# Kernel optimization log

Measured on AMD Instinct MI355X. Metric: run time of the kernel, lower is better.

Reference implementation:

```python
import jax, jax.numpy as jnp
import numpy as np

B, S, D, H, F, M = 2, 2048, 1024, 16, 4096, 1024
HD = D // H
LR, MOM_DECAY, WD, THRESH = 0.01, 0.9, 0.01, 0.1


def rmsnorm(x, w, eps=1e-8):
    n = jnp.linalg.norm(x, axis=-1, keepdims=True) * (x.shape[-1] ** -0.5)
    return w * x / (n + eps)


def rope_sin_cos(seq_len, dim):
    inv_freq = 1.0 / (10000.0 ** (jnp.arange(0, dim, 2, dtype=jnp.float32) / dim))
    ang = jnp.arange(seq_len, dtype=jnp.float32)[:, None] * inv_freq[None, :]  # [S, dim/2]
    return jnp.sin(ang), jnp.cos(ang)


def apply_rope(x, sin, cos):
    # x: [B,H,S,hd]; sin/cos: [S,hd/2] broadcast. Matches torch source:
    # split even/odd lanes, then CONCATENATE halves (not interleave).
    x1, x2 = x[..., ::2], x[..., 1::2]
    return jnp.concatenate([x1 * cos - x2 * sin, x1 * sin + x2 * cos], axis=-1)


def lmm_mlp(z, w0, b0, w1, b1):
    return jnp.maximum(z @ w0 + b0, 0.0) @ w1 + b1


def setup_inputs() -> dict:
    key = jax.random.key(0)
    k = jax.random.split(key, 20)
    sc = 0.02
    r = lambda i, shape: jax.random.normal(k[i], shape, jnp.float32) * sc
    return {
        'x': jax.random.normal(k[0], (B, S, D), jnp.float32),
        'mask': jnp.tril(jnp.ones((1, 1, S, S), dtype=bool)),
        'wq': r(1, (D, D)), 'wk': r(2, (D, D)), 'wv': r(3, (D, D)), 'wo': r(4, (D, D)),
        'n1': jnp.ones(D, jnp.float32), 'n2': jnp.ones(D, jnp.float32), 'n3': jnp.ones(D, jnp.float32),
        'ffn_w1': r(5, (D, F)), 'ffn_w2': r(6, (D, F)), 'ffn_w3': r(7, (F, D)),
        'pk_w': r(8, (D, M)), 'pk_b': jnp.zeros(M, jnp.float32),
        'pv_w': r(9, (D, M)), 'pv_b': jnp.zeros(M, jnp.float32),
        'pq_w': r(10, (D, M)), 'pq_b': jnp.zeros(M, jnp.float32),
        'l0_w': r(11, (M, M)), 'l0_b': jnp.zeros(M, jnp.float32),
        'l1_w': r(12, (M, M)), 'l1_b': jnp.zeros(M, jnp.float32),
        'm0_w': jnp.zeros((M, M), jnp.float32), 'm0_b': jnp.zeros(M, jnp.float32),
        'm1_w': jnp.zeros((M, M), jnp.float32), 'm1_b': jnp.zeros(M, jnp.float32),
    }


def reference(x, mask, wq, wk, wv, wo, n1, n2, n3, ffn_w1, ffn_w2, ffn_w3,
              pk_w, pk_b, pv_w, pv_b, pq_w, pq_b,
              l0_w, l0_b, l1_w, l1_b, m0_w, m0_b, m1_w, m1_b):
    # ---- attention sublayer (pre-norm, RoPE) ----
    hn = rmsnorm(x, n1)
    q = (hn @ wq).reshape(B, S, H, HD).transpose(0, 2, 1, 3)
    kk = (hn @ wk).reshape(B, S, H, HD).transpose(0, 2, 1, 3)
    v = (hn @ wv).reshape(B, S, H, HD).transpose(0, 2, 1, 3)
    sin, cos = rope_sin_cos(S, HD)
    q = apply_rope(q, sin, cos)
    kk = apply_rope(kk, sin, cos)
    scores = jnp.einsum('bhqd,bhkd->bhqk', q, kk) / np.sqrt(HD).astype(np.float32)
    scores = jnp.where(mask, scores, -jnp.inf)
    attn = jax.nn.softmax(scores, axis=-1)
    o = jnp.einsum('bhqk,bhkd->bhqd', attn, v).transpose(0, 2, 1, 3).reshape(B, S, D)
    h = x + o @ wo

    # ---- neural memory sublayer ----
    hn2 = rmsnorm(h, n2)
    q_lmm = hn2 @ pq_w + pq_b
    retrieved = lmm_mlp(q_lmm, l0_w, l0_b, l1_w, l1_b)  # uses PRE-update params

    # online Titan-style LMM update (torch does this under no_grad, after retrieval)
    kf = jax.lax.stop_gradient((hn2 @ pk_w + pk_b).reshape(B * S, M))
    vf = jax.lax.stop_gradient((hn2 @ pv_w + pv_b).reshape(B * S, M))

    def lmm_loss(params):
        pred = lmm_mlp(kf, *params)
        return jnp.sum(jnp.mean((pred - vf) ** 2, axis=-1))

    params = (l0_w, l0_b, l1_w, l1_b)
    loss_sum, grads = jax.value_and_grad(lmm_loss)(params)
    avg_loss = loss_sum / (B * S)
    do_update = avg_loss >= THRESH
    moms = (m0_w, m0_b, m1_w, m1_b)
    new_moms, new_params = [], []
    for p, m, g in zip(params, moms, grads):
        nm = MOM_DECAY * m - LR * g
        np_ = p * (1.0 - WD) + nm
        new_moms.append(jnp.where(do_update, nm, m))
        new_params.append(jnp.where(do_update, np_, p))

    h = h + retrieved

    # ---- SwiGLU FFN sublayer ----
    hn3 = rmsnorm(h, n3)
    ffn = (jax.nn.silu(hn3 @ ffn_w1) * (hn3 @ ffn_w2)) @ ffn_w3
    out = h + ffn
    return (out, *new_params, *new_moms)
```

## Files before the change

kernel.cpp:

```cpp
#include <hip/hip_runtime.h>
#include <cstdint>
#include <cstddef>

typedef __bf16 bf16;
typedef __bf16 bf16x2 __attribute__((ext_vector_type(2)));
typedef __bf16 bf16x4 __attribute__((ext_vector_type(4)));
typedef __bf16 bf16x8 __attribute__((ext_vector_type(8)));
typedef float  f32x4  __attribute__((ext_vector_type(4)));
typedef float  f32x16 __attribute__((ext_vector_type(16)));
typedef __attribute__((address_space(1))) unsigned int u32_g;
typedef __attribute__((address_space(3))) unsigned int u32_l;

#define DI __device__ __forceinline__

constexpr int Bc = 2, Sc = 2048, Dc = 1024, Hc = 16, HDc = 64, Fc = 4096, Mc = 1024;
constexpr int NTc = Bc * Sc;

DI void llds16(const bf16* g, bf16* l) {
  __builtin_amdgcn_global_load_lds((const u32_g*)g, (u32_l*)l, 16, 0, 0);
}
DI f32x4 cvt4(bf16x4 a) {
  f32x4 r; r[0] = (float)a[0]; r[1] = (float)a[1]; r[2] = (float)a[2]; r[3] = (float)a[3];
  return r;
}

__global__ void k_detect(const unsigned short* __restrict__ x, int* __restrict__ flag)
{
  const int tid = threadIdx.x;
  int cnt = 0;
#pragma unroll
  for (int i = 0; i < 8; i++) {
    unsigned short h = x[tid * 8 + i];
    int e = (h >> 7) & 0xFF;
    if (e < 96 || e > 160) cnt++;
  }
#pragma unroll
  for (int off = 32; off > 0; off >>= 1) cnt += __shfl_down(cnt, off, 64);
  if (tid == 0) *flag = (cnt > 32) ? 1 : 0;
}

__global__ __launch_bounds__(256)
void k_cvt(const void* __restrict__ src, bf16* __restrict__ dst, int n4, const int* __restrict__ flag)
{
  int i = blockIdx.x * 256 + threadIdx.x;
  if (i >= n4) return;
  bf16x4 o;
  if (*flag) {
    f32x4 v = ((const f32x4*)src)[i];
    o[0] = (bf16)v[0]; o[1] = (bf16)v[1]; o[2] = (bf16)v[2]; o[3] = (bf16)v[3];
  } else {
    o = ((const bf16x4*)src)[i];
  }
  ((bf16x4*)dst)[i] = o;
}

__global__ void k_transpose_dt(const void* __restrict__ src, bf16* __restrict__ dst,
                               int R, int C, const int* __restrict__ flag)
{
  __shared__ bf16 tile[32][33];
  const int c0 = blockIdx.x * 32, r0 = blockIdx.y * 32;
  const int tx = threadIdx.x, ty = threadIdx.y;
  const bool f32 = (*flag != 0);
  for (int i = ty; i < 32; i += 8) {
    size_t idx = (size_t)(r0 + i) * C + (c0 + tx);
    tile[i][tx] = f32 ? (bf16)((const float*)src)[idx] : ((const bf16*)src)[idx];
  }
  __syncthreads();
  for (int i = ty; i < 32; i += 8)
    dst[(size_t)(c0 + i) * R + (r0 + tx)] = tile[tx][i];
}

__global__ void k_transpose_v(const bf16* __restrict__ v, bf16* __restrict__ vt)
{
  __shared__ bf16 tile[32][33];
  const int d0 = blockIdx.x * 32, s0 = blockIdx.y * 32;
  const int bh = blockIdx.z;
  const int b = bh >> 4, hh = bh & 15;
  const int tx = threadIdx.x, ty = threadIdx.y;
  for (int i = ty; i < 32; i += 8)
    tile[i][tx] = v[((size_t)(b * Sc + s0 + i)) * Dc + hh * HDc + d0 + tx];
  __syncthreads();
  for (int i = ty; i < 32; i += 8)
    vt[((size_t)(bh * HDc + d0 + i)) * Sc + s0 + tx] = tile[tx][i];
}

enum EpiMode { EPI_BF16 = 0, EPI_BIAS_BF16, EPI_BIAS_RELU_BF16, EPI_BIAS_RESB_F32,
               EPI_SILU_BF16, EPI_DZ_BF16, EPI_RESX_BF16, EPI_RESF_F32,
               EPI_SEGC_BF16, EPI_SEGC_BIAS_BF16, EPI_SEG2_RELU_BF16, EPI_ATOMIC_F32 };

template <int EPI>
__global__ __launch_bounds__(256)
void k_gemm(const bf16* __restrict__ A, const bf16* __restrict__ Bt,
            int Mr, int Nr, int Kr,
            float* outF, bf16* outB,
            const bf16* __restrict__ bias, const bf16* auxB,
            const float* resF,
            const void* __restrict__ resX, const int* __restrict__ flag)
{
  __shared__ bf16 As[128 * 32];
  __shared__ bf16 Bs[128 * 32];
  const int tid = threadIdx.x;
  const int w = tid >> 6, l = tid & 63;
  const int wr = w >> 1, wc = w & 1;
  const int row0 = blockIdx.y * 128, col0 = blockIdx.x * 128;

  const f32x4 vzero = {0.f, 0.f, 0.f, 0.f};
  f32x4 acc[4][4];
#pragma unroll
  for (int i = 0; i < 4; i++)
#pragma unroll
    for (int j = 0; j < 4; j++) acc[i][j] = vzero;

  const bf16* Ag = A + (size_t)(row0 + w * 16 + (l >> 2)) * Kr + ((l & 3) << 3);
  const bf16* Bg = Bt + (size_t)(col0 + w * 16 + (l >> 2)) * Kr + ((l & 3) << 3);
  bf16* AsW = &As[w * 512];
  bf16* BsW = &Bs[w * 512];
  const size_t rowHop = (size_t)64 * Kr;

  const int chunk = Kr / gridDim.z;
  const int kbeg = blockIdx.z * chunk;

  for (int k0 = kbeg; k0 < kbeg + chunk; k0 += 32) {
    __syncthreads();
    llds16(Ag + k0, AsW);
    llds16(Ag + rowHop + k0, AsW + 2048);
    llds16(Bg + k0, BsW);
    llds16(Bg + rowHop + k0, BsW + 2048);
    __syncthreads();
    bf16x8 af[4], bfr[4];
#pragma unroll
    for (int mt = 0; mt < 4; mt++)
      af[mt] = *(const bf16x8*)&As[(wr * 64 + mt * 16 + (l & 15)) * 32 + (l >> 4) * 8];
#pragma unroll
    for (int nt = 0; nt < 4; nt++)
      bfr[nt] = *(const bf16x8*)&Bs[(wc * 64 + nt * 16 + (l & 15)) * 32 + (l >> 4) * 8];
#pragma unroll
    for (int mt = 0; mt < 4; mt++)
#pragma unroll
      for (int nt = 0; nt < 4; nt++)
        acc[mt][nt] = __builtin_amdgcn_mfma_f32_16x16x32_bf16(af[mt], bfr[nt], acc[mt][nt], 0, 0, 0);
  }

  const bool f32res = (EPI == EPI_RESX_BF16) ? (*flag != 0) : false;
  float biasv[4];
  if (EPI == EPI_BIAS_BF16 || EPI == EPI_BIAS_RELU_BF16 || EPI == EPI_BIAS_RESB_F32 ||
      EPI == EPI_SEGC_BIAS_BF16 || EPI == EPI_SEG2_RELU_BF16) {
#pragma unroll
    for (int nt = 0; nt < 4; nt++)
      biasv[nt] = (float)bias[col0 + wc * 64 + nt * 16 + (l & 15)];
  }
#pragma unroll
  for (int mt = 0; mt < 4; mt++) {
    const int rowb = row0 + wr * 64 + mt * 16 + ((l >> 4) << 2);
    float av[4][4];
    if (EPI == EPI_SILU_BF16 || EPI == EPI_DZ_BF16 || EPI == EPI_BIAS_RESB_F32) {
#pragma unroll
      for (int nt = 0; nt < 4; nt++) {
        const int col = col0 + wc * 64 + nt * 16 + (l & 15);
#pragma unroll
        for (int r = 0; r < 4; r++)
          av[nt][r] = (float)auxB[(size_t)(rowb + r) * Nr + col];
      }
    }
    if (EPI == EPI_RESF_F32) {
#pragma unroll
      for (int nt = 0; nt < 4; nt++) {
        const int col = col0 + wc * 64 + nt * 16 + (l & 15);
#pragma unroll
        for (int r = 0; r < 4; r++)
          av[nt][r] = resF[(size_t)(rowb + r) * Nr + col];
      }
    }
    if (EPI == EPI_RESX_BF16) {
#pragma unroll
      for (int nt = 0; nt < 4; nt++) {
        const int col = col0 + wc * 64 + nt * 16 + (l & 15);
#pragma unroll
        for (int r = 0; r < 4; r++) {
          const size_t idx = (size_t)(rowb + r) * Nr + col;
          av[nt][r] = f32res ? ((const float*)resX)[idx] : (float)((const bf16*)resX)[idx];
        }
      }
    }
#pragma unroll
    for (int nt = 0; nt < 4; nt++) {
      const int col = col0 + wc * 64 + nt * 16 + (l & 15);
#pragma unroll
      for (int r = 0; r < 4; r++) {
        const size_t idx = (size_t)(rowb + r) * Nr + col;
        float v = acc[mt][nt][r];
        if (EPI == EPI_BF16) { outB[idx] = (bf16)v; }
        else if (EPI == EPI_BIAS_BF16) { outB[idx] = (bf16)(v + biasv[nt]); }
        else if (EPI == EPI_BIAS_RELU_BF16) { outB[idx] = (bf16)fmaxf(v + biasv[nt], 0.f); }
        else if (EPI == EPI_BIAS_RESB_F32) { outF[idx] = v + biasv[nt] + av[nt][r]; }
        else if (EPI == EPI_SILU_BF16) {
          float s1v = av[nt][r];
          float sl = s1v / (1.f + __expf(-s1v));
          outB[idx] = (bf16)(sl * v);
        }
        else if (EPI == EPI_DZ_BF16) { outB[idx] = (bf16)(av[nt][r] > 0.f ? v : 0.f); }
        else if (EPI == EPI_RESX_BF16) { outB[idx] = (bf16)(v + av[nt][r]); }
        else if (EPI == EPI_RESF_F32) { outF[idx] = v + av[nt][r]; }
        else if (EPI == EPI_SEGC_BF16 || EPI == EPI_SEGC_BIAS_BF16) {
          const size_t sidx = (size_t)(col >> 10) * ((size_t)NTc * 1024)
                            + (size_t)(rowb + r) * 1024 + (col & 1023);
          float vv = (EPI == EPI_SEGC_BIAS_BF16) ? (v + biasv[nt]) : v;
          outB[sidx] = (bf16)vv;
        }
        else if (EPI == EPI_SEG2_RELU_BF16) {
          bf16* ob = (rowb >> 12) ? (bf16*)outF : outB;
          ob[(size_t)((rowb + r) & 4095) * 1024 + col] = (bf16)fmaxf(v + biasv[nt], 0.f);
        }
        else if (EPI == EPI_ATOMIC_F32) {
          atomicAdd(&outF[(size_t)(rowb + r) * Nr + col], v);
        }
      }
    }
  }
}

__global__ __launch_bounds__(256)
void k_gemm_tn(const bf16* __restrict__ X, const bf16* __restrict__ Y, int Kt,
               float* __restrict__ out)
{
  __shared__ bf16 As[128 * 36];
  __shared__ bf16 Bs[128 * 36];
  const int tid = threadIdx.x;
  const int w = tid >> 6, l = tid & 63;
  const int wr = w >> 1, wc = w & 1;
  const int row0 = blockIdx.y * 128, col0 = blockIdx.x * 128;
  const int iofs = (tid & 15) * 8;
  const int tp   = (tid >> 4) * 2;

  const f32x4 vzero = {0.f, 0.f, 0.f, 0.f};
  f32x4 acc[4][4];
#pragma unroll
  for (int i = 0; i < 4; i++)
#pragma unroll
    for (int j = 0; j < 4; j++) acc[i][j] = vzero;

  const int chunk = Kt / gridDim.z;
  const int tbeg = blockIdx.z * chunk;

  for (int t0 = tbeg; t0 < tbeg + chunk; t0 += 32) {
    __syncthreads();
    bf16x8 a0 = *(const bf16x8*)&X[(size_t)(t0 + tp) * 1024 + row0 + iofs];
    bf16x8 a1 = *(const bf16x8*)&X[(size_t)(t0 + tp + 1) * 1024 + row0 + iofs];
    bf16x8 b0 = *(const bf16x8*)&Y[(size_t)(t0 + tp) * 1024 + col0 + iofs];
    bf16x8 b1 = *(const bf16x8*)&Y[(size_t)(t0 + tp + 1) * 1024 + col0 + iofs];
#pragma unroll
    for (int e = 0; e < 8; e++) {
      bf16x2 pa; pa[0] = a0[e]; pa[1] = a1[e];
      bf16x2 pb; pb[0] = b0[e]; pb[1] = b1[e];
      *(bf16x2*)&As[(iofs + e) * 36 + tp] = pa;
      *(bf16x2*)&Bs[(iofs + e) * 36 + tp] = pb;
    }
    __syncthreads();
    bf16x8 af[4], bfr[4];
#pragma unroll
    for (int mt = 0; mt < 4; mt++) {
      const int base = (wr * 64 + mt * 16 + (l & 15)) * 36 + (l >> 4) * 8;
      bf16x4 lo = *(const bf16x4*)&As[base];
      bf16x4 hi = *(const bf16x4*)&As[base + 4];
#pragma unroll
      for (int e = 0; e < 4; e++) { af[mt][e] = lo[e]; af[mt][4 + e] = hi[e]; }
    }
#pragma unroll
    for (int nt = 0; nt < 4; nt++) {
      const int base = (wc * 64 + nt * 16 + (l & 15)) * 36 + (l >> 4) * 8;
      bf16x4 lo = *(const bf16x4*)&Bs[base];
      bf16x4 hi = *(const bf16x4*)&Bs[base + 4];
#pragma unroll
      for (int e = 0; e < 4; e++) { bfr[nt][e] = lo[e]; bfr[nt][4 + e] = hi[e]; }
    }
#pragma unroll
    for (int mt = 0; mt < 4; mt++)
#pragma unroll
      for (int nt = 0; nt < 4; nt++)
        acc[mt][nt] = __builtin_amdgcn_mfma_f32_16x16x32_bf16(af[mt], bfr[nt], acc[mt][nt], 0, 0, 0);
  }

#pragma unroll
  for (int mt = 0; mt < 4; mt++) {
    const int rowb = row0 + wr * 64 + mt * 16 + ((l >> 4) << 2);
#pragma unroll
    for (int nt = 0; nt < 4; nt++) {
      const int col = col0 + wc * 64 + nt * 16 + (l & 15);
#pragma unroll
      for (int r = 0; r < 4; r++)
        atomicAdd(&out[(size_t)(rowb + r) * 1024 + col], acc[mt][nt][r]);
    }
  }
}

__global__ __launch_bounds__(256)
void k_rmsnorm_dt(const void* __restrict__ x, const bf16* __restrict__ w, bf16* __restrict__ out,
                  const int* __restrict__ flag)
{
  const int row = blockIdx.x;
  const int tid = threadIdx.x;
  f32x4 xv;
  if (*flag) xv = *(const f32x4*)((const float*)x + (size_t)row * Dc + tid * 4);
  else       xv = cvt4(*(const bf16x4*)((const bf16*)x + (size_t)row * Dc + tid * 4));
  float ss = xv[0] * xv[0] + xv[1] * xv[1] + xv[2] * xv[2] + xv[3] * xv[3];
#pragma unroll
  for (int off = 32; off > 0; off >>= 1) ss += __shfl_down(ss, off, 64);
  __shared__ float part[4];
  if ((tid & 63) == 0) part[tid >> 6] = ss;
  __syncthreads();
  float tot = part[0] + part[1] + part[2] + part[3];
  float inv = 1.f / (sqrtf(tot) * 0.03125f + 1e-8f);
  bf16x4 wb = *(const bf16x4*)(w + tid * 4);
  bf16x4 ov;
  ov[0] = (bf16)((float)wb[0] * xv[0] * inv);
  ov[1] = (bf16)((float)wb[1] * xv[1] * inv);
  ov[2] = (bf16)((float)wb[2] * xv[2] * inv);
  ov[3] = (bf16)((float)wb[3] * xv[3] * inv);
  *(bf16x4*)(out + (size_t)row * Dc + tid * 4) = ov;
}

__global__ __launch_bounds__(256)
void k_rmsnorm_b(const bf16* __restrict__ x, const bf16* __restrict__ w, bf16* __restrict__ out)
{
  const int row = blockIdx.x;
  const int tid = threadIdx.x;
  f32x4 xv = cvt4(*(const bf16x4*)(x + (size_t)row * Dc + tid * 4));
  float ss = xv[0] * xv[0] + xv[1] * xv[1] + xv[2] * xv[2] + xv[3] * xv[3];
#pragma unroll
  for (int off = 32; off > 0; off >>= 1) ss += __shfl_down(ss, off, 64);
  __shared__ float part[4];
  if ((tid & 63) == 0) part[tid >> 6] = ss;
  __syncthreads();
  float tot = part[0] + part[1] + part[2] + part[3];
  float inv = 1.f / (sqrtf(tot) * 0.03125f + 1e-8f);
  bf16x4 wb = *(const bf16x4*)(w + tid * 4);
  bf16x4 ov;
  ov[0] = (bf16)((float)wb[0] * xv[0] * inv);
  ov[1] = (bf16)((float)wb[1] * xv[1] * inv);
  ov[2] = (bf16)((float)wb[2] * xv[2] * inv);
  ov[3] = (bf16)((float)wb[3] * xv[3] * inv);
  *(bf16x4*)(out + (size_t)row * Dc + tid * 4) = ov;
}

__global__ __launch_bounds__(256)
void k_rmsnorm_f(const float* __restrict__ x, const bf16* __restrict__ w, bf16* __restrict__ out)
{
  const int row = blockIdx.x;
  const int tid = threadIdx.x;
  f32x4 xv = *(const f32x4*)(x + (size_t)row * Dc + tid * 4);
  float ss = xv[0] * xv[0] + xv[1] * xv[1] + xv[2] * xv[2] + xv[3] * xv[3];
#pragma unroll
  for (int off = 32; off > 0; off >>= 1) ss += __shfl_down(ss, off, 64);
  __shared__ float part[4];
  if ((tid & 63) == 0) part[tid >> 6] = ss;
  __syncthreads();
  float tot = part[0] + part[1] + part[2] + part[3];
  float inv = 1.f / (sqrtf(tot) * 0.03125f + 1e-8f);
  bf16x4 wb = *(const bf16x4*)(w + tid * 4);
  bf16x4 ov;
  ov[0] = (bf16)((float)wb[0] * xv[0] * inv);
  ov[1] = (bf16)((float)wb[1] * xv[1] * inv);
  ov[2] = (bf16)((float)wb[2] * xv[2] * inv);
  ov[3] = (bf16)((float)wb[3] * xv[3] * inv);
  *(bf16x4*)(out + (size_t)row * Dc + tid * 4) = ov;
}

__global__ __launch_bounds__(256)
void k_rope(bf16* __restrict__ q, bf16* __restrict__ kx)
{
  const int idx = blockIdx.x * 256 + threadIdx.x;
  const int t = idx >> 4, hh = idx & 15;
  const int s = t & (Sc - 1);
  float sn[32], cs[32];
#pragma unroll
  for (int i = 0; i < 32; i++) {
    float f = expf(-(float)i * 0.28782313662425574f);
    float ang = (float)s * f;
    sn[i] = sinf(ang);
    cs[i] = cosf(ang);
  }
  for (int pass = 0; pass < 2; pass++) {
    bf16* p = (pass ? kx : q) + (size_t)t * Dc + hh * HDc;
    float xb[64], ob[64];
#pragma unroll
    for (int j = 0; j < 16; j++) *(f32x4*)&xb[j * 4] = cvt4(*(const bf16x4*)(p + j * 4));
#pragma unroll
    for (int i = 0; i < 32; i++) {
      float x1 = xb[2 * i], x2 = xb[2 * i + 1];
      ob[i] = x1 * cs[i] - x2 * sn[i];
      ob[32 + i] = x1 * sn[i] + x2 * cs[i];
    }
#pragma unroll
    for (int j = 0; j < 16; j++) {
      bf16x4 o4;
      o4[0] = (bf16)ob[j * 4]; o4[1] = (bf16)ob[j * 4 + 1];
      o4[2] = (bf16)ob[j * 4 + 2]; o4[3] = (bf16)ob[j * 4 + 3];
      *(bf16x4*)(p + j * 4) = o4;
    }
  }
}

__global__ __launch_bounds__(256)
void k_attn(const bf16* __restrict__ q, const bf16* __restrict__ kx,
            const bf16* __restrict__ vt, bf16* __restrict__ o)
{
  union UV { bf16x8 v; unsigned int u[4]; };
  union UH { bf16x2 h; unsigned int u; };

  const int blk = blockIdx.x;
  const int g  = 15 - (blk >> 5);
  const int bh = blk & 31;
  const int b = bh >> 4, hh = bh & 15;
  const int tid = threadIdx.x;
  const int w = tid >> 6, l = tid & 63;
  const int hi = l >> 5, lq = l & 31;

  const int q0 = g * 128 + w * 32;
  const int ntiles = g * 4 + w + 1;

  const bf16* kb = kx + (size_t)b * Sc * Dc + hh * HDc;
  const bf16* vb = vt + (size_t)bh * HDc * Sc;

  bf16x8 qf[4];
  {
    const bf16* qp = q + ((size_t)(b * Sc + q0 + lq)) * Dc + hh * HDc + hi * 8;
#pragma unroll
    for (int ds = 0; ds < 4; ds++) {
      qf[ds] = *(const bf16x8*)(qp + ds * 16);
#pragma unroll
      for (int j = 0; j < 8; j++) qf[ds][j] = (bf16)((float)qf[ds][j] * 0.125f);
    }
  }

  f32x16 oacc0, oacc1;
#pragma unroll
  for (int j = 0; j < 16; j++) { oacc0[j] = 0.f; oacc1[j] = 0.f; }
  float mrun = -3.0e38f, lrun = 0.f;

  for (int t0 = 0; t0 < ntiles; t0++) {
    const int kk0 = t0 * 32;

    const bf16* kp = kb + (size_t)(kk0 + lq) * Dc + hi * 8;
    f32x16 sacc;
#pragma unroll
    for (int j = 0; j < 16; j++) sacc[j] = 0.f;
#pragma unroll
    for (int ds = 0; ds < 4; ds++) {
      bf16x8 kf = *(const bf16x8*)(kp + ds * 16);
      sacc = __builtin_amdgcn_mfma_f32_32x32x16_bf16(kf, qf[ds], sacc, 0, 0, 0);
    }

    if (t0 == ntiles - 1) {
#pragma unroll
      for (int reg = 0; reg < 16; reg++) {
        const int kidx = (reg & 3) + 8 * (reg >> 2) + 4 * hi;
        sacc[reg] = (kidx > lq) ? -3.0e38f : sacc[reg];
      }
    }

    float mx = sacc[0];
#pragma unroll
    for (int reg = 1; reg < 16; reg++) mx = fmaxf(mx, sacc[reg]);
    mx = fmaxf(mx, __shfl_xor(mx, 32, 64));

    const float mnew = fmaxf(mrun, mx);
    const float al = __expf(mrun - mnew);
    mrun = mnew;
    float p[16], ps = 0.f;
#pragma unroll
    for (int reg = 0; reg < 16; reg++) { p[reg] = __expf(sacc[reg] - mnew); ps += p[reg]; }
    ps += __shfl_xor(ps, 32, 64);
    lrun = lrun * al + ps;
#pragma unroll
    for (int j = 0; j < 16; j++) { oacc0[j] *= al; oacc1[j] *= al; }

    unsigned int wv[8];
#pragma unroll
    for (int m = 0; m < 8; m++) {
      UH t; t.h[0] = (bf16)p[2 * m]; t.h[1] = (bf16)p[2 * m + 1];
      wv[m] = t.u;
    }
    const unsigned int ex0 = __shfl_xor(hi ? wv[0] : wv[2], 32, 64);
    const unsigned int ex1 = __shfl_xor(hi ? wv[1] : wv[3], 32, 64);
    const unsigned int ex2 = __shfl_xor(hi ? wv[4] : wv[6], 32, 64);
    const unsigned int ex3 = __shfl_xor(hi ? wv[5] : wv[7], 32, 64);
    UV pa0, pa1;
    pa0.u[0] = hi ? ex0 : wv[0];  pa0.u[1] = hi ? ex1 : wv[1];
    pa0.u[2] = hi ? wv[2] : ex0;  pa0.u[3] = hi ? wv[3] : ex1;
    pa1.u[0] = hi ? ex2 : wv[4];  pa1.u[1] = hi ? ex3 : wv[5];
    pa1.u[2] = hi ? wv[6] : ex2;  pa1.u[3] = hi ? wv[7] : ex3;

    const bf16* vp = vb + (size_t)lq * Sc + kk0 + hi * 8;
    bf16x8 v00 = *(const bf16x8*)(vp);
    bf16x8 v10 = *(const bf16x8*)(vp + 16);
    bf16x8 v01 = *(const bf16x8*)(vp + (size_t)32 * Sc);
    bf16x8 v11 = *(const bf16x8*)(vp + (size_t)32 * Sc + 16);
    oacc0 = __builtin_amdgcn_mfma_f32_32x32x16_bf16(v00, pa0.v, oacc0, 0, 0, 0);
    oacc0 = __builtin_amdgcn_mfma_f32_32x32x16_bf16(v10, pa1.v, oacc0, 0, 0, 0);
    oacc1 = __builtin_amdgcn_mfma_f32_32x32x16_bf16(v01, pa0.v, oacc1, 0, 0, 0);
    oacc1 = __builtin_amdgcn_mfma_f32_32x32x16_bf16(v11, pa1.v, oacc1, 0, 0, 0);
  }

  const float inv = 1.f / lrun;
  bf16* op = o + ((size_t)(b * Sc + q0 + lq)) * Dc + hh * HDc;
#pragma unroll
  for (int m = 0; m < 8; m++) {
    const int d0 = (2 * m & 3) + 8 * (m >> 1) + 4 * hi;
    UH t0v; t0v.h[0] = (bf16)(oacc0[2 * m] * inv); t0v.h[1] = (bf16)(oacc0[2 * m + 1] * inv);
    *(unsigned int*)(op + d0) = t0v.u;
    UH t1v; t1v.h[0] = (bf16)(oacc1[2 * m] * inv); t1v.h[1] = (bf16)(oacc1[2 * m + 1] * inv);
    *(unsigned int*)(op + 32 + d0) = t1v.u;
  }
}

__global__ __launch_bounds__(256)
void k_dpred(bf16* __restrict__ predDp, const bf16* __restrict__ vf, float* __restrict__ loss)
{
  __shared__ float red[4];
  const int tid = threadIdx.x;
  const size_t n8 = (size_t)NTc * Mc / 8;
  float lacc = 0.f;
  for (size_t i = (size_t)blockIdx.x * 256 + tid; i < n8; i += (size_t)gridDim.x * 256) {
    bf16x8 p8 = ((const bf16x8*)predDp)[i];
    bf16x8 v8 = ((const bf16x8*)vf)[i];
    bf16x8 d8;
#pragma unroll
    for (int e = 0; e < 8; e++) {
      float df = (float)p8[e] - (float)v8[e];
      lacc += df * df;
      d8[e] = (bf16)(df * (2.0f / 1024.0f));
    }
    ((bf16x8*)predDp)[i] = d8;
  }
#pragma unroll
  for (int off = 32; off > 0; off >>= 1) lacc += __shfl_down(lacc, off, 64);
  if ((tid & 63) == 0) red[tid >> 6] = lacc;
  __syncthreads();
  if (tid == 0) atomicAdd(loss, red[0] + red[1] + red[2] + red[3]);
}

__global__ __launch_bounds__(256)
void k_colsum(const bf16* __restrict__ X, float* __restrict__ out, int C, int rowsPer)
{
  int c = blockIdx.x * 256 + threadIdx.x;
  int r0 = blockIdx.y * rowsPer;
  float s = 0.f;
#pragma unroll 8
  for (int r = r0; r < r0 + rowsPer; r++) s += (float)X[(size_t)r * C + c];
  atomicAdd(&out[c], s);
}

__global__ __launch_bounds__(256)
void k_update_dt(const void* __restrict__ p0w, const void* __restrict__ p0b,
                 const void* __restrict__ p1w, const void* __restrict__ p1b,
                 const void* __restrict__ m0w, const void* __restrict__ m0b,
                 const void* __restrict__ m1w, const void* __restrict__ m1b,
                 const float* __restrict__ g0wF, const float* __restrict__ g0b,
                 const float* __restrict__ g1wF, const float* __restrict__ g1b,
                 const float* __restrict__ loss, const int* __restrict__ flag,
                 float* __restrict__ outP, float* __restrict__ outM)
{
  const int i = blockIdx.x * 256 + threadIdx.x;
  const bool upd = (loss[0] >= 0.1f * 1024.f * 4096.f);
  const bool f32 = (*flag != 0);
  constexpr int W = 1024 * 1024;
  const void *pp, *pm; int j; float g;
  if (i < W) { pp = p0w; pm = m0w; j = i; g = g0wF[i]; }
  else if (i < W + 1024) { j = i - W; pp = p0b; pm = m0b; g = g0b[j]; }
  else if (i < 2 * W + 1024) { j = i - W - 1024; pp = p1w; pm = m1w; g = g1wF[j]; }
  else { j = i - 2 * W - 1024; pp = p1b; pm = m1b; g = g1b[j]; }
  float p = f32 ? ((const float*)pp)[j] : (float)((const bf16*)pp)[j];
  float m = f32 ? ((const float*)pm)[j] : (float)((const bf16*)pm)[j];
  float nm = 0.9f * m - 0.01f * g;
  float np = 0.99f * p + nm;
  outP[i] = upd ? np : p;
  outM[i] = upd ? nm : m;
}

extern "C" void kernel_launch(void* const* d_in, const int* in_sizes, int n_in,
                              void* d_out, int out_size, void* d_ws, size_t ws_size,
                              hipStream_t stream)
{
  (void)in_sizes; (void)n_in; (void)out_size; (void)ws_size;
  const void* x   = d_in[0];
  const void* wq  = d_in[2];
  const void* wk  = d_in[3];
  const void* wv  = d_in[4];
  const void* wo  = d_in[5];
  const void* n1  = d_in[6];
  const void* n2  = d_in[7];
  const void* n3  = d_in[8];
  const void* fw1 = d_in[9];
  const void* fw2 = d_in[10];
  const void* fw3 = d_in[11];
  const void* pkw = d_in[12];
  const void* pkb = d_in[13];
  const void* pvw = d_in[14];
  const void* pvb = d_in[15];
  const void* pqw = d_in[16];
  const void* pqb = d_in[17];
  const void* l0w = d_in[18];
  const void* l0b = d_in[19];
  const void* l1w = d_in[20];
  const void* l1b = d_in[21];
  const void* m0w = d_in[22];
  const void* m0b = d_in[23];
  const void* m1w = d_in[24];
  const void* m1b = d_in[25];

  char* ws = (char*)d_ws;
  size_t off = 0;
  auto alloc = [&](size_t bytes) -> char* {
    char* p = ws + off;
    off += (bytes + 255) & ~(size_t)255;
    return p;
  };

  const size_t DD = (size_t)Dc * Dc;
  const size_t ND = (size_t)NTc * Dc;
  const size_t MB8 = 2 * ND;
  const size_t M1 = DD;

  bf16* W = (bf16*)alloc(2 * 8 * M1);
  bf16 *wqT = W, *wkT = W + M1, *wvT = W + 2 * M1, *woT = W + 3 * M1;
  bf16 *pqT = W + 4 * M1, *pkT = W + 5 * M1, *pvT = W + 6 * M1, *l0T = W + 7 * M1;
  bf16 *l1T = W + M1;
  bf16 *h1buf = W + 2 * M1;
  bf16 *l1c = W;
  bf16 *w1T = W + 4 * M1;
  bf16 *w2T = W;
  bf16 *w3T = W + 4 * M1;

  bf16* B0 = (bf16*)alloc(MB8);
  bf16* B1 = (bf16*)alloc(MB8);
  bf16* B2 = (bf16*)alloc(MB8);
  bf16* B3 = (bf16*)alloc(MB8);
  bf16* B4 = (bf16*)alloc(MB8);
  bf16* s1 = B0;
  bf16* VtG = B4;

  float* g0b = (float*)alloc(4 * 1024);
  float* g1b = (float*)alloc(4 * 1024);
  float* lossb = (float*)alloc(256);
  int*   flag  = (int*)alloc(256);
  bf16* n1c = (bf16*)alloc(2 * 1024);
  bf16* n2c = (bf16*)alloc(2 * 1024);
  bf16* n3c = (bf16*)alloc(2 * 1024);
  bf16* bqkv = (bf16*)alloc(2 * 3072);
  bf16* b0c = (bf16*)alloc(2 * 1024);
  bf16* b1c = (bf16*)alloc(2 * 1024);

  float* outX = (float*)d_out;
  float* outP = outX + ND;
  float* outM = outP + (2 * DD + 2048);
  float* g0wF = outM;
  float* g1wF = outM + M1 + 1024;
  bf16*  hn   = (bf16*)outX;

  const dim3 tb(32, 8);

  hipMemsetAsync(lossb, 0, sizeof(float), stream);
  hipMemsetAsync(g0b, 0, 4 * 1024, stream);
  hipMemsetAsync(g1b, 0, 4 * 1024, stream);
  hipMemsetAsync(outM, 0, (2 * M1 + 2048) * sizeof(float), stream);
  k_detect<<<1, 64, 0, stream>>>((const unsigned short*)x, flag);

  k_cvt<<<1, 256, 0, stream>>>(n1, n1c, 256, flag);
  k_cvt<<<1, 256, 0, stream>>>(n2, n2c, 256, flag);
  k_cvt<<<1, 256, 0, stream>>>(n3, n3c, 256, flag);
  k_cvt<<<1, 256, 0, stream>>>(pqb, bqkv, 256, flag);
  k_cvt<<<1, 256, 0, stream>>>(pkb, bqkv + 1024, 256, flag);
  k_cvt<<<1, 256, 0, stream>>>(pvb, bqkv + 2048, 256, flag);
  k_cvt<<<1, 256, 0, stream>>>(l0b, b0c, 256, flag);
  k_cvt<<<1, 256, 0, stream>>>(l1b, b1c, 256, flag);

  k_transpose_dt<<<dim3(32, 32), tb, 0, stream>>>(wq, wqT, Dc, Dc, flag);
  k_transpose_dt<<<dim3(32, 32), tb, 0, stream>>>(wk, wkT, Dc, Dc, flag);
  k_transpose_dt<<<dim3(32, 32), tb, 0, stream>>>(wv, wvT, Dc, Dc, flag);
  k_transpose_dt<<<dim3(32, 32), tb, 0, stream>>>(wo, woT, Dc, Dc, flag);
  k_transpose_dt<<<dim3(32, 32), tb, 0, stream>>>(pqw, pqT, Dc, Mc, flag);
  k_transpose_dt<<<dim3(32, 32), tb, 0, stream>>>(pkw, pkT, Dc, Mc, flag);
  k_transpose_dt<<<dim3(32, 32), tb, 0, stream>>>(pvw, pvT, Dc, Mc, flag);
  k_transpose_dt<<<dim3(32, 32), tb, 0, stream>>>(l0w, l0T, Mc, Mc, flag);

  k_rmsnorm_dt<<<NTc, 256, 0, stream>>>(x, n1c, hn, flag);
  k_gemm<EPI_SEGC_BF16><<<dim3(24, 32), 256, 0, stream>>>(hn, wqT, NTc, 3072, Dc, nullptr, B0, nullptr, nullptr, nullptr, nullptr, nullptr);
  k_transpose_v<<<dim3(2, 64, 32), tb, 0, stream>>>(B2, VtG);
  k_rope<<<256, 256, 0, stream>>>(B0, B1);
  k_attn<<<512, 256, 0, stream>>>(B0, B1, VtG, B3);
  k_gemm<EPI_RESX_BF16><<<dim3(8, 32), 256, 0, stream>>>(B3, woT, NTc, Dc, Dc, nullptr, B4, nullptr, nullptr, nullptr, x, flag);
  k_transpose_dt<<<dim3(32, 32), tb, 0, stream>>>(l1w, l1T, Mc, Mc, flag);

  k_rmsnorm_b<<<NTc, 256, 0, stream>>>(B4, n2c, B0);
  k_gemm<EPI_SEGC_BIAS_BF16><<<dim3(24, 32), 256, 0, stream>>>(B0, pqT, NTc, 3072, Dc, nullptr, B1, bqkv, nullptr, nullptr, nullptr, nullptr);
  k_gemm<EPI_SEG2_RELU_BF16><<<dim3(8, 64), 256, 0, stream>>>(B1, l0T, 2 * NTc, Mc, Mc, (float*)h1buf, B0, b0c, nullptr, nullptr, nullptr, nullptr);
  k_gemm<EPI_BIAS_RESB_F32><<<dim3(8, 32), 256, 0, stream>>>(B0, l1T, NTc, Mc, Mc, outX, nullptr, b1c, B4, nullptr, nullptr, nullptr);
  k_gemm<EPI_BIAS_BF16><<<dim3(8, 32), 256, 0, stream>>>(h1buf, l1T, NTc, Mc, Mc, nullptr, B1, b1c, nullptr, nullptr, nullptr, nullptr);

  k_cvt<<<1024, 256, 0, stream>>>(l1w, l1c, (int)(DD / 4), flag);
  k_dpred<<<256, 256, 0, stream>>>(B1, B3, lossb);
  k_gemm<EPI_DZ_BF16><<<dim3(8, 32), 256, 0, stream>>>(B1, l1c, NTc, Mc, Mc, nullptr, B3, nullptr, h1buf, nullptr, nullptr, nullptr);
  k_gemm_tn<<<dim3(8, 8, 8), 256, 0, stream>>>(h1buf, B1, NTc, g1wF);
  k_gemm_tn<<<dim3(8, 8, 8), 256, 0, stream>>>(B2, B3, NTc, g0wF);
  k_transpose_dt<<<dim3(128, 32), tb, 0, stream>>>(fw1, w1T, Dc, Fc, flag);
  k_colsum<<<dim3(4, 32), 256, 0, stream>>>(B1, g1b, Mc, NTc / 32);
  k_colsum<<<dim3(4, 32), 256, 0, stream>>>(B3, g0b, Mc, NTc / 32);
  k_update_dt<<<8200, 256, 0, stream>>>(l0w, l0b, l1w, l1b, m0w, m0b, m1w, m1b,
                                        g0wF, g0b, g1wF, g1b, lossb, flag, outP, outM);

  k_transpose_dt<<<dim3(128, 32), tb, 0, stream>>>(fw2, w2T, Dc, Fc, flag);
  k_rmsnorm_f<<<NTc, 256, 0, stream>>>(outX, n3c, B4);
  k_gemm<EPI_BF16><<<dim3(32, 32), 256, 0, stream>>>(B4, w1T, NTc, Fc, Dc, nullptr, s1, nullptr, nullptr, nullptr, nullptr, nullptr);
  k_transpose_dt<<<dim3(32, 128), tb, 0, stream>>>(fw3, w3T, Fc, Dc, flag);
  k_gemm<EPI_SILU_BF16><<<dim3(32, 32), 256, 0, stream>>>(B4, w2T, NTc, Fc, Dc, nullptr, s1, nullptr, s1, nullptr, nullptr, nullptr);
  k_gemm<EPI_ATOMIC_F32><<<dim3(8, 32, 2), 256, 0, stream>>>(s1, w3T, NTc, Dc, Fc, outX, nullptr, nullptr, nullptr, nullptr, nullptr, nullptr);
}
```

Before: 954.1 us.

## Split attention KV loop across warps with shared-memory softmax merge

```diff
diff --git a/kernel.cpp b/kernel.cpp
--- a/kernel.cpp
+++ b/kernel.cpp
@@ -407,16 +407,18 @@
   union UV { bf16x8 v; unsigned int u[4]; };
   union UH { bf16x2 h; unsigned int u; };
 
+  __shared__ float Buf[3 * 64 * 35];
+
   const int blk = blockIdx.x;
-  const int g  = 15 - (blk >> 5);
+  const int qc = 63 - (blk >> 5);
   const int bh = blk & 31;
   const int b = bh >> 4, hh = bh & 15;
   const int tid = threadIdx.x;
   const int w = tid >> 6, l = tid & 63;
   const int hi = l >> 5, lq = l & 31;
 
-  const int q0 = g * 128 + w * 32;
-  const int ntiles = g * 4 + w + 1;
+  const int q0 = qc * 32;
+  const int ntiles = qc + 1;
 
   const bf16* kb = kx + (size_t)b * Sc * Dc + hh * HDc;
   const bf16* vb = vt + (size_t)bh * HDc * Sc;
@@ -437,7 +439,7 @@
   for (int j = 0; j < 16; j++) { oacc0[j] = 0.f; oacc1[j] = 0.f; }
   float mrun = -3.0e38f, lrun = 0.f;
 
-  for (int t0 = 0; t0 < ntiles; t0++) {
+  for (int t0 = w; t0 < ntiles; t0 += 4) {
     const int kk0 = t0 * 32;
 
     const bf16* kp = kb + (size_t)(kk0 + lq) * Dc + hi * 8;
@@ -501,15 +503,40 @@
     oacc1 = __builtin_amdgcn_mfma_f32_32x32x16_bf16(v11, pa1.v, oacc1, 0, 0, 0);
   }
 
-  const float inv = 1.f / lrun;
-  bf16* op = o + ((size_t)(b * Sc + q0 + lq)) * Dc + hh * HDc;
-#pragma unroll
-  for (int m = 0; m < 8; m++) {
-    const int d0 = (2 * m & 3) + 8 * (m >> 1) + 4 * hi;
-    UH t0v; t0v.h[0] = (bf16)(oacc0[2 * m] * inv); t0v.h[1] = (bf16)(oacc0[2 * m + 1] * inv);
-    *(unsigned int*)(op + d0) = t0v.u;
-    UH t1v; t1v.h[0] = (bf16)(oacc1[2 * m] * inv); t1v.h[1] = (bf16)(oacc1[2 * m + 1] * inv);
-    *(unsigned int*)(op + 32 + d0) = t1v.u;
+  if (w > 0) {
+    float* dst = &Buf[((w - 1) * 64 + l) * 35];
+#pragma unroll
+    for (int j = 0; j < 16; j++) { dst[j] = oacc0[j]; dst[16 + j] = oacc1[j]; }
+    dst[32] = mrun; dst[33] = lrun;
+  }
+  __syncthreads();
+  if (w == 0) {
+#pragma unroll
+    for (int w2 = 0; w2 < 3; w2++) {
+      const float* src = &Buf[(w2 * 64 + l) * 35];
+      const float m2 = src[32], l2 = src[33];
+      const float mn = fmaxf(mrun, m2);
+      const float a = __expf(mrun - mn);
+      const float bb = __expf(m2 - mn);
+      lrun = lrun * a + l2 * bb;
+      mrun = mn;
+#pragma unroll
+      for (int j = 0; j < 16; j++) {
+        oacc0[j] = oacc0[j] * a + src[j] * bb;
+        oacc1[j] = oacc1[j] * a + src[16 + j] * bb;
+      }
+    }
+
+    const float inv = 1.f / lrun;
+    bf16* op = o + ((size_t)(b * Sc + q0 + lq)) * Dc + hh * HDc;
+#pragma unroll
+    for (int m = 0; m < 8; m++) {
+      const int d0 = (2 * m & 3) + 8 * (m >> 1) + 4 * hi;
+      UH t0v; t0v.h[0] = (bf16)(oacc0[2 * m] * inv); t0v.h[1] = (bf16)(oacc0[2 * m + 1] * inv);
+      *(unsigned int*)(op + d0) = t0v.u;
+      UH t1v; t1v.h[0] = (bf16)(oacc1[2 * m] * inv); t1v.h[1] = (bf16)(oacc1[2 * m + 1] * inv);
+      *(unsigned int*)(op + 32 + d0) = t1v.u;
+    }
   }
 }
 
@@ -687,7 +714,7 @@
   k_gemm<EPI_SEGC_BF16><<<dim3(24, 32), 256, 0, stream>>>(hn, wqT, NTc, 3072, Dc, nullptr, B0, nullptr, nullptr, nullptr, nullptr, nullptr);
   k_transpose_v<<<dim3(2, 64, 32), tb, 0, stream>>>(B2, VtG);
   k_rope<<<256, 256, 0, stream>>>(B0, B1);
-  k_attn<<<512, 256, 0, stream>>>(B0, B1, VtG, B3);
+  k_attn<<<2048, 256, 0, stream>>>(B0, B1, VtG, B3);
   k_gemm<EPI_RESX_BF16><<<dim3(8, 32), 256, 0, stream>>>(B3, woT, NTc, Dc, Dc, nullptr, B4, nullptr, nullptr, nullptr, x, flag);
   k_transpose_dt<<<dim3(32, 32), tb, 0, stream>>>(l1w, l1T, Mc, Mc, flag);
 
```

Result: faster. 921.3 us (-3.4%).
